# Kernel optimization log

Hardware: AMD Instinct MI355X
Metric: run time of the kernel (lower is better)

Reference implementation:

```python
import jax, jax.numpy as jnp
import numpy as np

NO_URLS = 2000
D = 256  # sen_emb_size * 2
B, S = 16, 256


def setup_inputs() -> dict:
    key = jax.random.key(0)
    k1, k2, k3, k4 = jax.random.split(key, 4)
    inp = jax.random.normal(k1, (B, S, D), dtype=jnp.float32)
    urls = jax.random.randint(k2, (B, S), 0, NO_URLS, dtype=jnp.int32)
    # params ~ U(-1, 1) as in random_()
    trans = jax.random.uniform(k3, (NO_URLS, D, D), dtype=jnp.float32, minval=-1.0, maxval=1.0)
    bias = jax.random.uniform(k4, (NO_URLS, D), dtype=jnp.float32, minval=-1.0, maxval=1.0)
    return {"input": inp, "urls": urls, "trans": trans, "bias": bias}


def reference(input, urls, trans, bias):
    # input: [B, S, D], urls: [B, S], trans: [U, D, D], bias: [U, D]
    b, s, d = input.shape
    x = input.reshape(-1, d)          # [N, D], N = B*S
    u = urls.reshape(-1)              # [N]
    # per-token gathered matvec + bias (vectorized form of the python loop)
    out = jnp.einsum('nd,nde->ne', x, trans[u]) + bias[u]
    return jnp.tanh(out).reshape(input.shape)
```

## Files before the change

### kernel.cpp

```cpp
#include <hip/hip_runtime.h>
#include <math.h>

#define N_TOK 4096
#define DIM   256
#define NURL  2000
#define TCH   4

#define WS_COUNTS 0
#define WS_OFFS   2048
#define WS_CURS   4096
#define WS_BUCKET 6144

__global__ __launch_bounds__(256) void zero_k(int* __restrict__ ws) {
    const int i = blockIdx.x * 256 + threadIdx.x;
    if (i < NURL) ws[WS_COUNTS + i] = 0;
}

__global__ __launch_bounds__(256) void hist_k(const int* __restrict__ urls,
                                              int* __restrict__ ws) {
    const int n = blockIdx.x * 256 + threadIdx.x;
    atomicAdd(&ws[WS_COUNTS + urls[n]], 1);
}

__global__ __launch_bounds__(64) void scan_k(int* __restrict__ ws) {
    const int lane = threadIdx.x;
    const int base = lane * 32;
    int c[32];
    int local = 0;
#pragma unroll
    for (int i = 0; i < 32; ++i) {
        const int u = base + i;
        c[i] = (u < NURL) ? ws[WS_COUNTS + u] : 0;
        local += c[i];
    }
    int x = local;
    for (int off = 1; off < 64; off <<= 1) {
        const int y = __shfl_up(x, off);
        if (lane >= off) x += y;
    }
    int run = x - local;
#pragma unroll
    for (int i = 0; i < 32; ++i) {
        const int u = base + i;
        if (u < NURL) { ws[WS_OFFS + u] = run; ws[WS_CURS + u] = run; }
        run += c[i];
    }
}

__global__ __launch_bounds__(256) void scatter_k(const int* __restrict__ urls,
                                                 int* __restrict__ ws) {
    const int n = blockIdx.x * 256 + threadIdx.x;
    const int u = urls[n];
    const int pos = atomicAdd(&ws[WS_CURS + u], 1);
    ws[WS_BUCKET + pos] = n;
}

#define FMA4(acc, xv, tv)                 \
    acc.x = fmaf((xv), (tv).x, acc.x);    \
    acc.y = fmaf((xv), (tv).y, acc.y);    \
    acc.z = fmaf((xv), (tv).z, acc.z);    \
    acc.w = fmaf((xv), (tv).w, acc.w);

__global__ __launch_bounds__(256) void compute_k(
    const float* __restrict__ inp,
    const float* __restrict__ trans,
    const float* __restrict__ bias,
    const int*   __restrict__ ws,
    float*       __restrict__ out)
{
    const int u   = blockIdx.x;
    const int cnt = ws[WS_COUNTS + u];
    if (cnt == 0) return;
    const int start = ws[WS_OFFS + u];
    const int tid  = threadIdx.x;
    const int wave = tid >> 6;
    const int lane = tid & 63;

    __shared__ __align__(16) float xs[TCH][DIM];
    __shared__ __align__(16) float part[4][TCH][DIM];
    __shared__ __align__(16) float bs[DIM];
    __shared__ int toks[TCH];

    if (tid < 64) {
        reinterpret_cast<float4*>(bs)[tid] =
            reinterpret_cast<const float4*>(bias + (size_t)u * DIM)[tid];
    }

    const float4* T4 =
        reinterpret_cast<const float4*>(trans + (size_t)u * DIM * DIM) + lane;

    for (int c0 = 0; c0 < cnt; c0 += TCH) {
        const int nk = min(TCH, cnt - c0);

        if (tid < nk * 64) {
            const int k = tid >> 6, l = tid & 63;
            const int tok = ws[WS_BUCKET + start + c0 + k];
            if (l == 0) toks[k] = tok;
            reinterpret_cast<float4*>(xs[k])[l] =
                reinterpret_cast<const float4*>(inp + (size_t)tok * DIM)[l];
        }
        __syncthreads();

        float4 a0 = {0,0,0,0}, a1 = {0,0,0,0}, a2 = {0,0,0,0}, a3 = {0,0,0,0};
        const int dbase = wave * 64;
#pragma unroll 2
        for (int d0 = 0; d0 < 64; d0 += 4) {
            const int d = dbase + d0;
            const float4 x0 = *reinterpret_cast<const float4*>(&xs[0][d]);
            const float4 x1 = *reinterpret_cast<const float4*>(&xs[1][d]);
            const float4 x2 = *reinterpret_cast<const float4*>(&xs[2][d]);
            const float4 x3 = *reinterpret_cast<const float4*>(&xs[3][d]);
            const float4 t0 = T4[(size_t)(d + 0) * (DIM / 4)];
            const float4 t1 = T4[(size_t)(d + 1) * (DIM / 4)];
            const float4 t2 = T4[(size_t)(d + 2) * (DIM / 4)];
            const float4 t3 = T4[(size_t)(d + 3) * (DIM / 4)];
            FMA4(a0, x0.x, t0) FMA4(a0, x0.y, t1) FMA4(a0, x0.z, t2) FMA4(a0, x0.w, t3)
            FMA4(a1, x1.x, t0) FMA4(a1, x1.y, t1) FMA4(a1, x1.z, t2) FMA4(a1, x1.w, t3)
            FMA4(a2, x2.x, t0) FMA4(a2, x2.y, t1) FMA4(a2, x2.z, t2) FMA4(a2, x2.w, t3)
            FMA4(a3, x3.x, t0) FMA4(a3, x3.y, t1) FMA4(a3, x3.z, t2) FMA4(a3, x3.w, t3)
        }

        reinterpret_cast<float4*>(part[wave][0])[lane] = a0;
        reinterpret_cast<float4*>(part[wave][1])[lane] = a1;
        reinterpret_cast<float4*>(part[wave][2])[lane] = a2;
        reinterpret_cast<float4*>(part[wave][3])[lane] = a3;
        __syncthreads();

        if (wave < nk) {
            const float4 p0 = reinterpret_cast<const float4*>(part[0][wave])[lane];
            const float4 p1 = reinterpret_cast<const float4*>(part[1][wave])[lane];
            const float4 p2 = reinterpret_cast<const float4*>(part[2][wave])[lane];
            const float4 p3 = reinterpret_cast<const float4*>(part[3][wave])[lane];
            const float4 b4 = reinterpret_cast<const float4*>(bs)[lane];
            float4 o;
            o.x = tanhf(p0.x + p1.x + p2.x + p3.x + b4.x);
            o.y = tanhf(p0.y + p1.y + p2.y + p3.y + b4.y);
            o.z = tanhf(p0.z + p1.z + p2.z + p3.z + b4.z);
            o.w = tanhf(p0.w + p1.w + p2.w + p3.w + b4.w);
            reinterpret_cast<float4*>(out + (size_t)toks[wave] * DIM)[lane] = o;
        }
        __syncthreads();
    }
}

extern "C" void kernel_launch(void* const* d_in, const int* in_sizes, int n_in,
                              void* d_out, int out_size, void* d_ws, size_t ws_size,
                              hipStream_t stream) {
    const float* inp   = (const float*)d_in[0];
    const int*   urls  = (const int*)  d_in[1];
    const float* trans = (const float*)d_in[2];
    const float* bias  = (const float*)d_in[3];
    float*       out   = (float*)d_out;
    int*         ws    = (int*)d_ws;

    zero_k<<<(NURL + 255) / 256, 256, 0, stream>>>(ws);
    hist_k<<<N_TOK / 256, 256, 0, stream>>>(urls, ws);
    scan_k<<<1, 64, 0, stream>>>(ws);
    scatter_k<<<N_TOK / 256, 256, 0, stream>>>(urls, ws);
    compute_k<<<NURL, 256, 0, stream>>>(inp, trans, bias, ws, out);
}
```

Baseline: 678.3 us.

## Pair two URLs per block and split each matrix across two waves

Each block now serves two URLs, with two waves per URL. Each wave covers 128 rows of the transform instead of 64 and processes up to 8 tokens per chunk instead of 4. The grid is halved, the per-URL bias is kept in registers, and the cross-wave reduction shrinks to a pairwise sum through shared memory. The aim is to reuse each loaded transform row across more tokens and to cut reduction and sync overhead. The cost is longer serial load chains per wave and fewer waves in flight overall, which may reduce memory-level parallelism.

```diff
diff --git a/kernel.cpp b/kernel.cpp
--- a/kernel.cpp
+++ b/kernel.cpp
@@ -4,7 +4,7 @@
 #define N_TOK 4096
 #define DIM   256
 #define NURL  2000
-#define TCH   4
+#define TCH   8
 
 #define WS_COUNTS 0
 #define WS_OFFS   2048
@@ -68,76 +68,99 @@
     const int*   __restrict__ ws,
     float*       __restrict__ out)
 {
-    const int u   = blockIdx.x;
-    const int cnt = ws[WS_COUNTS + u];
-    if (cnt == 0) return;
-    const int start = ws[WS_OFFS + u];
     const int tid  = threadIdx.x;
     const int wave = tid >> 6;
     const int lane = tid & 63;
+    const int wq   = wave >> 1;
+    const int half = wave & 1;
 
-    __shared__ __align__(16) float xs[TCH][DIM];
-    __shared__ __align__(16) float part[4][TCH][DIM];
-    __shared__ __align__(16) float bs[DIM];
-    __shared__ int toks[TCH];
+    const int cntA = ws[WS_COUNTS + 2 * blockIdx.x + 0];
+    const int cntB = ws[WS_COUNTS + 2 * blockIdx.x + 1];
+    const int nch  = max((cntA + TCH - 1) / TCH, (cntB + TCH - 1) / TCH);
+    if (nch == 0) return;
 
-    if (tid < 64) {
-        reinterpret_cast<float4*>(bs)[tid] =
-            reinterpret_cast<const float4*>(bias + (size_t)u * DIM)[tid];
-    }
+    const int u     = 2 * blockIdx.x + wq;
+    const int cnt   = (wq == 0) ? cntA : cntB;
+    const int start = ws[WS_OFFS + u];
 
+    __shared__ __align__(16) float xs[2][TCH][DIM];
+    __shared__ __align__(16) float part[2][TCH][DIM];
+    __shared__ int toks[2][TCH];
+
+    const float4 bv = reinterpret_cast<const float4*>(bias + (size_t)u * DIM)[lane];
     const float4* T4 =
         reinterpret_cast<const float4*>(trans + (size_t)u * DIM * DIM) + lane;
+    const int dbase = half * 128;
 
-    for (int c0 = 0; c0 < cnt; c0 += TCH) {
-        const int nk = min(TCH, cnt - c0);
+    for (int c = 0; c < nch; ++c) {
+        const int nk = min(TCH, cnt - c * TCH);
 
-        if (tid < nk * 64) {
-            const int k = tid >> 6, l = tid & 63;
-            const int tok = ws[WS_BUCKET + start + c0 + k];
-            if (l == 0) toks[k] = tok;
-            reinterpret_cast<float4*>(xs[k])[l] =
-                reinterpret_cast<const float4*>(inp + (size_t)tok * DIM)[l];
+#pragma unroll
+        for (int k = 0; k < 4; ++k) {
+            const int kk = half * 4 + k;
+            if (kk < nk) {
+                const int tok = ws[WS_BUCKET + start + c * TCH + kk];
+                reinterpret_cast<float4*>(xs[wq][kk])[lane] =
+                    reinterpret_cast<const float4*>(inp + (size_t)tok * DIM)[lane];
+                if (lane == 0) toks[wq][kk] = tok;
+            }
         }
         __syncthreads();
 
         float4 a0 = {0,0,0,0}, a1 = {0,0,0,0}, a2 = {0,0,0,0}, a3 = {0,0,0,0};
-        const int dbase = wave * 64;
-#pragma unroll 2
-        for (int d0 = 0; d0 < 64; d0 += 4) {
-            const int d = dbase + d0;
-            const float4 x0 = *reinterpret_cast<const float4*>(&xs[0][d]);
-            const float4 x1 = *reinterpret_cast<const float4*>(&xs[1][d]);
-            const float4 x2 = *reinterpret_cast<const float4*>(&xs[2][d]);
-            const float4 x3 = *reinterpret_cast<const float4*>(&xs[3][d]);
-            const float4 t0 = T4[(size_t)(d + 0) * (DIM / 4)];
-            const float4 t1 = T4[(size_t)(d + 1) * (DIM / 4)];
-            const float4 t2 = T4[(size_t)(d + 2) * (DIM / 4)];
-            const float4 t3 = T4[(size_t)(d + 3) * (DIM / 4)];
-            FMA4(a0, x0.x, t0) FMA4(a0, x0.y, t1) FMA4(a0, x0.z, t2) FMA4(a0, x0.w, t3)
-            FMA4(a1, x1.x, t0) FMA4(a1, x1.y, t1) FMA4(a1, x1.z, t2) FMA4(a1, x1.w, t3)
-            FMA4(a2, x2.x, t0) FMA4(a2, x2.y, t1) FMA4(a2, x2.z, t2) FMA4(a2, x2.w, t3)
-            FMA4(a3, x3.x, t0) FMA4(a3, x3.y, t1) FMA4(a3, x3.z, t2) FMA4(a3, x3.w, t3)
+        float4 a4 = {0,0,0,0}, a5 = {0,0,0,0}, a6 = {0,0,0,0}, a7 = {0,0,0,0};
+
+        if (nk > 0) {
+            const float* xw = &xs[wq][0][0];
+#pragma unroll 8
+            for (int d0 = 0; d0 < 128; ++d0) {
+                const int d = dbase + d0;
+                const float4 tv = T4[(size_t)d * (DIM / 4)];
+                const float x0 = xw[0 * DIM + d];
+                const float x1 = xw[1 * DIM + d];
+                const float x2 = xw[2 * DIM + d];
+                const float x3 = xw[3 * DIM + d];
+                const float x4 = xw[4 * DIM + d];
+                const float x5 = xw[5 * DIM + d];
+                const float x6 = xw[6 * DIM + d];
+                const float x7 = xw[7 * DIM + d];
+                FMA4(a0, x0, tv) FMA4(a1, x1, tv) FMA4(a2, x2, tv) FMA4(a3, x3, tv)
+                FMA4(a4, x4, tv) FMA4(a5, x5, tv) FMA4(a6, x6, tv) FMA4(a7, x7, tv)
+            }
+
+            if (half == 0) {
+                reinterpret_cast<float4*>(part[wq][4])[lane] = a4;
+                reinterpret_cast<float4*>(part[wq][5])[lane] = a5;
+                reinterpret_cast<float4*>(part[wq][6])[lane] = a6;
+                reinterpret_cast<float4*>(part[wq][7])[lane] = a7;
+            } else {
+                reinterpret_cast<float4*>(part[wq][0])[lane] = a0;
+                reinterpret_cast<float4*>(part[wq][1])[lane] = a1;
+                reinterpret_cast<float4*>(part[wq][2])[lane] = a2;
+                reinterpret_cast<float4*>(part[wq][3])[lane] = a3;
+            }
         }
-
-        reinterpret_cast<float4*>(part[wave][0])[lane] = a0;
-        reinterpret_cast<float4*>(part[wave][1])[lane] = a1;
-        reinterpret_cast<float4*>(part[wave][2])[lane] = a2;
-        reinterpret_cast<float4*>(part[wave][3])[lane] = a3;
         __syncthreads();
 
-        if (wave < nk) {
-            const float4 p0 = reinterpret_cast<const float4*>(part[0][wave])[lane];
-            const float4 p1 = reinterpret_cast<const float4*>(part[1][wave])[lane];
-            const float4 p2 = reinterpret_cast<const float4*>(part[2][wave])[lane];
-            const float4 p3 = reinterpret_cast<const float4*>(part[3][wave])[lane];
-            const float4 b4 = reinterpret_cast<const float4*>(bs)[lane];
-            float4 o;
-            o.x = tanhf(p0.x + p1.x + p2.x + p3.x + b4.x);
-            o.y = tanhf(p0.y + p1.y + p2.y + p3.y + b4.y);
-            o.z = tanhf(p0.z + p1.z + p2.z + p3.z + b4.z);
-            o.w = tanhf(p0.w + p1.w + p2.w + p3.w + b4.w);
-            reinterpret_cast<float4*>(out + (size_t)toks[wave] * DIM)[lane] = o;
+        if (nk > 0) {
+            if (half == 0) {
+#define FIN(K, ACC)                                                            \
+                if ((K) < nk) {                                                \
+                    const float4 p =                                           \
+                        reinterpret_cast<const float4*>(part[wq][K])[lane];    \
+                    float4 o;                                                  \
+                    o.x = tanhf(ACC.x + p.x + bv.x);                           \
+                    o.y = tanhf(ACC.y + p.y + bv.y);                           \
+                    o.z = tanhf(ACC.z + p.z + bv.z);                           \
+                    o.w = tanhf(ACC.w + p.w + bv.w);                           \
+                    reinterpret_cast<float4*>(                                 \
+                        out + (size_t)toks[wq][K] * DIM)[lane] = o;            \
+                }
+                FIN(0, a0) FIN(1, a1) FIN(2, a2) FIN(3, a3)
+            } else {
+                FIN(4, a4) FIN(5, a5) FIN(6, a6) FIN(7, a7)
+#undef FIN
+            }
         }
         __syncthreads();
     }
@@ -157,5 +180,5 @@
     hist_k<<<N_TOK / 256, 256, 0, stream>>>(urls, ws);
     scan_k<<<1, 64, 0, stream>>>(ws);
     scatter_k<<<N_TOK / 256, 256, 0, stream>>>(urls, ws);
-    compute_k<<<NURL, 256, 0, stream>>>(inp, trans, bias, ws, out);
+    compute_k<<<NURL / 2, 256, 0, stream>>>(inp, trans, bias, ws, out);
 }
```

Measured after the change: 718.6 us. +5.9%, slower.

## Switch from per-URL blocks to per-token single-wave blocks with XCD-aware ordering

Applied to the files above, without the earlier changes.

Replaces the per-URL compute kernel, which had 256 threads, split-K partials and a shared-memory reduction, with one 64-thread block per token. Each block walks the sorted bucket list and computes the full 256-long matvec. Block indices are swizzled so that tokens sharing a URL, which sit next to each other in the sorted bucket, land on the same XCD, where they can reuse the trans matrix through the shared L2. This drops the cross-wave reduction and the syncs and spreads work over 4096 blocks, but it gives up explicit reuse of trans rows across tokens inside a block. Reuse now depends on cache hits.

```diff
diff --git a/kernel.cpp b/kernel.cpp
--- a/kernel.cpp
+++ b/kernel.cpp
@@ -4,7 +4,6 @@
 #define N_TOK 4096
 #define DIM   256
 #define NURL  2000
-#define TCH   4
 
 #define WS_COUNTS 0
 #define WS_OFFS   2048
@@ -55,92 +54,45 @@
     ws[WS_BUCKET + pos] = n;
 }
 
-#define FMA4(acc, xv, tv)                 \
-    acc.x = fmaf((xv), (tv).x, acc.x);    \
-    acc.y = fmaf((xv), (tv).y, acc.y);    \
-    acc.z = fmaf((xv), (tv).z, acc.z);    \
-    acc.w = fmaf((xv), (tv).w, acc.w);
-
-__global__ __launch_bounds__(256) void compute_k(
+__global__ __launch_bounds__(64) void compute_tok(
     const float* __restrict__ inp,
+    const int*   __restrict__ urls,
     const float* __restrict__ trans,
     const float* __restrict__ bias,
     const int*   __restrict__ ws,
     float*       __restrict__ out)
 {
-    const int u   = blockIdx.x;
-    const int cnt = ws[WS_COUNTS + u];
-    if (cnt == 0) return;
-    const int start = ws[WS_OFFS + u];
-    const int tid  = threadIdx.x;
-    const int wave = tid >> 6;
-    const int lane = tid & 63;
+    const int b    = blockIdx.x;
+    const int work = ((b & 7) << 9) | (b >> 3);
+    const int n    = ws[WS_BUCKET + work];
+    const int t    = threadIdx.x;
+    const int u    = urls[n];
 
-    __shared__ __align__(16) float xs[TCH][DIM];
-    __shared__ __align__(16) float part[4][TCH][DIM];
-    __shared__ __align__(16) float bs[DIM];
-    __shared__ int toks[TCH];
+    __shared__ float xs[DIM];
+    reinterpret_cast<float4*>(xs)[t] =
+        reinterpret_cast<const float4*>(inp + (size_t)n * DIM)[t];
+    __syncthreads();
 
-    if (tid < 64) {
-        reinterpret_cast<float4*>(bs)[tid] =
-            reinterpret_cast<const float4*>(bias + (size_t)u * DIM)[tid];
+    const float4* T4 = reinterpret_cast<const float4*>(
+                           trans + (size_t)u * DIM * DIM) + t;
+    float4 acc = reinterpret_cast<const float4*>(bias + (size_t)u * DIM)[t];
+
+#pragma unroll 8
+    for (int d = 0; d < DIM; ++d) {
+        const float  x  = xs[d];
+        const float4 tv = T4[(size_t)d * (DIM / 4)];
+        acc.x = fmaf(x, tv.x, acc.x);
+        acc.y = fmaf(x, tv.y, acc.y);
+        acc.z = fmaf(x, tv.z, acc.z);
+        acc.w = fmaf(x, tv.w, acc.w);
     }
 
-    const float4* T4 =
-        reinterpret_cast<const float4*>(trans + (size_t)u * DIM * DIM) + lane;
-
-    for (int c0 = 0; c0 < cnt; c0 += TCH) {
-        const int nk = min(TCH, cnt - c0);
-
-        if (tid < nk * 64) {
-            const int k = tid >> 6, l = tid & 63;
-            const int tok = ws[WS_BUCKET + start + c0 + k];
-            if (l == 0) toks[k] = tok;
-            reinterpret_cast<float4*>(xs[k])[l] =
-                reinterpret_cast<const float4*>(inp + (size_t)tok * DIM)[l];
-        }
-        __syncthreads();
-
-        float4 a0 = {0,0,0,0}, a1 = {0,0,0,0}, a2 = {0,0,0,0}, a3 = {0,0,0,0};
-        const int dbase = wave * 64;
-#pragma unroll 2
-        for (int d0 = 0; d0 < 64; d0 += 4) {
-            const int d = dbase + d0;
-            const float4 x0 = *reinterpret_cast<const float4*>(&xs[0][d]);
-            const float4 x1 = *reinterpret_cast<const float4*>(&xs[1][d]);
-            const float4 x2 = *reinterpret_cast<const float4*>(&xs[2][d]);
-            const float4 x3 = *reinterpret_cast<const float4*>(&xs[3][d]);
-            const float4 t0 = T4[(size_t)(d + 0) * (DIM / 4)];
-            const float4 t1 = T4[(size_t)(d + 1) * (DIM / 4)];
-            const float4 t2 = T4[(size_t)(d + 2) * (DIM / 4)];
-            const float4 t3 = T4[(size_t)(d + 3) * (DIM / 4)];
-            FMA4(a0, x0.x, t0) FMA4(a0, x0.y, t1) FMA4(a0, x0.z, t2) FMA4(a0, x0.w, t3)
-            FMA4(a1, x1.x, t0) FMA4(a1, x1.y, t1) FMA4(a1, x1.z, t2) FMA4(a1, x1.w, t3)
-            FMA4(a2, x2.x, t0) FMA4(a2, x2.y, t1) FMA4(a2, x2.z, t2) FMA4(a2, x2.w, t3)
-            FMA4(a3, x3.x, t0) FMA4(a3, x3.y, t1) FMA4(a3, x3.z, t2) FMA4(a3, x3.w, t3)
-        }
-
-        reinterpret_cast<float4*>(part[wave][0])[lane] = a0;
-        reinterpret_cast<float4*>(part[wave][1])[lane] = a1;
-        reinterpret_cast<float4*>(part[wave][2])[lane] = a2;
-        reinterpret_cast<float4*>(part[wave][3])[lane] = a3;
-        __syncthreads();
-
-        if (wave < nk) {
-            const float4 p0 = reinterpret_cast<const float4*>(part[0][wave])[lane];
-            const float4 p1 = reinterpret_cast<const float4*>(part[1][wave])[lane];
-            const float4 p2 = reinterpret_cast<const float4*>(part[2][wave])[lane];
-            const float4 p3 = reinterpret_cast<const float4*>(part[3][wave])[lane];
-            const float4 b4 = reinterpret_cast<const float4*>(bs)[lane];
-            float4 o;
-            o.x = tanhf(p0.x + p1.x + p2.x + p3.x + b4.x);
-            o.y = tanhf(p0.y + p1.y + p2.y + p3.y + b4.y);
-            o.z = tanhf(p0.z + p1.z + p2.z + p3.z + b4.z);
-            o.w = tanhf(p0.w + p1.w + p2.w + p3.w + b4.w);
-            reinterpret_cast<float4*>(out + (size_t)toks[wave] * DIM)[lane] = o;
-        }
-        __syncthreads();
-    }
+    float4 o;
+    o.x = tanhf(acc.x);
+    o.y = tanhf(acc.y);
+    o.z = tanhf(acc.z);
+    o.w = tanhf(acc.w);
+    reinterpret_cast<float4*>(out + (size_t)n * DIM)[t] = o;
 }
 
 extern "C" void kernel_launch(void* const* d_in, const int* in_sizes, int n_in,
@@ -157,5 +109,5 @@
     hist_k<<<N_TOK / 256, 256, 0, stream>>>(urls, ws);
     scan_k<<<1, 64, 0, stream>>>(ws);
     scatter_k<<<N_TOK / 256, 256, 0, stream>>>(urls, ws);
-    compute_k<<<NURL, 256, 0, stream>>>(inp, trans, bias, ws, out);
+    compute_tok<<<N_TOK, 64, 0, stream>>>(inp, urls, trans, bias, ws, out);
 }
```

Measured after the change: 674.0 us. About the same (-0.6%).
